# Performance work log

Measured on AMD Instinct MI355X. Metric: run time of the kernel, lower is better.

Reference implementation:

```python
import jax, jax.numpy as jnp
import numpy as np

B, S, E = 2, 4096, 2560
H, HKV, D = 8, 4, 256
WINDOW = 1024
SOFTCAP = 50.0
SCALING = 256.0 ** -0.5  # query_pre_attn_scalar = 256
EPS = 1e-6
MASK_VAL = -2.3819763e38


def rms_norm(x, w):
    # RMSNorm with add_unit_offset=True, computed in float32
    xf = x.astype(jnp.float32)
    out = xf * jax.lax.rsqrt(jnp.mean(xf * xf, axis=-1, keepdims=True) + EPS)
    return (out * (1.0 + w.astype(jnp.float32))).astype(x.dtype)


def apply_rotary_emb(x, cos, sin):
    # x: [B, S, h, D]; cos/sin: [S, D/2]; half-split rotation
    x1, x2 = jnp.split(x, 2, axis=-1)
    c = cos[None, :, None, :]
    s = sin[None, :, None, :]
    return jnp.concatenate([x1 * c - x2 * s, x2 * c + x1 * s], axis=-1)


def setup_inputs() -> dict:
    key = jax.random.key(0)
    ks = jax.random.split(key, 6)
    hidden_states = jax.random.normal(ks[0], (B, S, E), dtype=jnp.float32)
    # RoPE frequencies, theta=10000
    inv_freq = 1.0 / (10000.0 ** (np.arange(0, D, 2, dtype=np.float32) / D))
    t = np.arange(S, dtype=np.float32)
    freqs = np.outer(t, inv_freq)  # [S, D/2]
    freqs_cos = jnp.asarray(np.cos(freqs), dtype=jnp.float32)
    freqs_sin = jnp.asarray(np.sin(freqs), dtype=jnp.float32)
    kv_write_indices = jnp.arange(S, dtype=jnp.int32)
    k_cache = jnp.zeros((B, S, HKV, D), dtype=jnp.float32)
    v_cache = jnp.zeros((B, S, HKV, D), dtype=jnp.float32)
    # causal mask and causal+sliding-window mask (additive)
    i = np.arange(S)[:, None]
    j = np.arange(S)[None, :]
    causal = j <= i
    sliding = causal & ((i - j) < WINDOW)
    mask = jnp.asarray(np.where(causal, 0.0, MASK_VAL), dtype=jnp.float32)
    mask = jnp.broadcast_to(mask[None, None], (B, 1, S, S))
    local_mask = jnp.asarray(np.where(sliding, 0.0, MASK_VAL), dtype=jnp.float32)
    local_mask = jnp.broadcast_to(local_mask[None, None], (B, 1, S, S))
    w_qkv = jax.random.normal(ks[1], ((H + 2 * HKV) * D, E), dtype=jnp.float32) * (E ** -0.5)
    w_o = jax.random.normal(ks[2], (E, H * D), dtype=jnp.float32) * ((H * D) ** -0.5)
    q_norm_w = jnp.zeros((D,), dtype=jnp.float32)
    k_norm_w = jnp.zeros((D,), dtype=jnp.float32)
    return dict(hidden_states=hidden_states, freqs_cos=freqs_cos, freqs_sin=freqs_sin,
                kv_write_indices=kv_write_indices, k_cache=k_cache, v_cache=v_cache,
                mask=mask, local_mask=local_mask, w_qkv=w_qkv, w_o=w_o,
                q_norm_w=q_norm_w, k_norm_w=k_norm_w)


def reference(hidden_states, freqs_cos, freqs_sin, kv_write_indices, k_cache, v_cache,
              mask, local_mask, w_qkv, w_o, q_norm_w, k_norm_w):
    bsz, input_len, _ = hidden_states.shape
    qkv = jnp.einsum('bse,fe->bsf', hidden_states, w_qkv)
    xq, xk, xv = jnp.split(qkv, [H * D, H * D + HKV * D], axis=-1)
    xq = xq.reshape(bsz, input_len, H, D)
    xk = xk.reshape(bsz, input_len, HKV, D)
    xv = xv.reshape(bsz, input_len, HKV, D)
    # QK RMSNorm
    xq = rms_norm(xq, q_norm_w)
    xk = rms_norm(xk, k_norm_w)
    # RoPE
    xq = apply_rotary_emb(xq, freqs_cos, freqs_sin)
    xk = apply_rotary_emb(xk, freqs_cos, freqs_sin)
    # KV cache write
    k_cache = k_cache.at[:, kv_write_indices].set(xk)
    v_cache = v_cache.at[:, kv_write_indices].set(xv)
    kv_len = k_cache.shape[1]
    # GQA expand: [B, T, HKV, D] -> [B, T, H, D]
    nrep = H // HKV
    key = jnp.repeat(k_cache, nrep, axis=2)
    value = jnp.repeat(v_cache, nrep, axis=2)
    q = jnp.transpose(xq, (0, 2, 1, 3)) * SCALING   # [B, H, S, D]
    k = jnp.transpose(key, (0, 2, 1, 3))            # [B, H, T, D]
    v = jnp.transpose(value, (0, 2, 1, 3))
    scores = jnp.einsum('bhqd,bhkd->bhqk', q, k)
    # logit softcapping
    scores = jnp.tanh(scores / SOFTCAP) * SOFTCAP
    # attn_type == LOCAL_SLIDING -> use local (sliding-window) mask
    scores = scores + local_mask
    probs = jax.nn.softmax(scores.astype(jnp.float32), axis=-1).astype(q.dtype)
    out = jnp.einsum('bhqk,bhkd->bhqd', probs, v)
    out = jnp.transpose(out, (0, 2, 1, 3)).reshape(bsz, input_len, H * D)
    return jnp.einsum('bsf,ef->bse', out, w_o)
```

## Files before the change

kernel.cpp:

```cpp
#include <hip/hip_runtime.h>
#include <stdint.h>
#include <stddef.h>

#define B_    2
#define S_    4096
#define E_    2560
#define H_    8
#define HKV_  4
#define D_    256
#define F_    4096
#define HD_   2048
#define WIN_  1024

typedef __bf16 bf16;
typedef bf16  bf16x8 __attribute__((ext_vector_type(8)));
typedef bf16  bf16x4 __attribute__((ext_vector_type(4)));
typedef float f32x4  __attribute__((ext_vector_type(4)));
typedef uint32_t u32;

__device__ __forceinline__ void gl_lds16(const void* g, void* l) {
  __builtin_amdgcn_global_load_lds((const __attribute__((address_space(1))) void*)g,
                                   (__attribute__((address_space(3))) void*)l, 16, 0, 0);
}

__device__ __forceinline__ void bar_mf() {
  asm volatile("" ::: "memory");
  __builtin_amdgcn_s_barrier();
  asm volatile("" ::: "memory");
}

__device__ __forceinline__ u32 pkbf16(float a, float b) {
  union { bf16 h[2]; u32 u; } cv;
  cv.h[0] = (bf16)a; cv.h[1] = (bf16)b; return cv.u;
}

__global__ __launch_bounds__(256) void to_bf16_plain(const float* __restrict__ src,
                                                     bf16* __restrict__ dst, int n) {
  const int i = (blockIdx.x * 256 + threadIdx.x) * 8;
  if (i >= n) return;
  f32x4 a = *(const f32x4*)(src + i);
  f32x4 b = *(const f32x4*)(src + i + 4);
  bf16x8 o;
#pragma unroll
  for (int j = 0; j < 4; ++j) { o[j] = (bf16)a[j]; o[j + 4] = (bf16)b[j]; }
  *(bf16x8*)(dst + i) = o;
}

template <int EPI, int BN>
__global__ __launch_bounds__(512, 2) void gemm_8ph(
    const bf16* __restrict__ A, const bf16* __restrict__ Bw, int Kd, int NT,
    bf16* __restrict__ qo, bf16* __restrict__ ko, bf16* __restrict__ vto,
    float* __restrict__ C, int Nout, int row_base) {
  constexpr int NBH = BN / 128;
  constexpr int JT  = BN / 64;
  __shared__ bf16 Lds[2][2 + NBH][128 * 64];

  const int tid  = threadIdx.x;
  const int lane = tid & 63;
  const int wave = tid >> 6;
  const int wm   = wave >> 2;
  const int wn   = wave & 3;
  const int l16  = lane & 15;
  const int quad = lane >> 4;

  const int nwg  = gridDim.x * gridDim.y;
  const int obid = blockIdx.y * gridDim.x + blockIdx.x;
  const int bid  = (obid & 7) * (nwg >> 3) + (obid >> 3);
  const int mt   = bid / gridDim.x;
  const int ntl  = bid - mt * gridDim.x;
  const int row0 = mt * 256, col0 = ntl * BN;

  const bf16* Ah[2] = {A + (size_t)row0 * Kd, A + (size_t)(row0 + 128) * Kd};
  const bf16* Bh[2] = {Bw + (size_t)col0 * Kd,
                       Bw + (size_t)(col0 + (NBH == 2 ? 128 : 0)) * Kd};

  auto stage = [&](int dbf, int hf, const bf16* src, int k0) {
#pragma unroll
    for (int i = 0; i < 2; ++i) {
      const int g = tid + i * 512;
      const int r = g >> 3, c = g & 7;
      gl_lds16(src + (size_t)r * Kd + k0 + ((c ^ (r & 7)) << 3),
               &Lds[dbf][hf][0] + g * 8);
    }
  };
  auto rdA = [&](int dbf, int i, int ks) -> bf16x8 {
    const int r = i * 16 + l16;
    return *(const bf16x8*)&Lds[dbf][wm][r * 64 + (((ks * 4 + quad) ^ (r & 7)) << 3)];
  };
  auto rdB = [&](int dbf, int j, int ks) -> bf16x8 {
    const int colt = wn * (BN / 4) + j * 16 + l16;
    const int r = colt & 127;
    return *(const bf16x8*)&Lds[dbf][2 + (colt >> 7)][r * 64 + (((ks * 4 + quad) ^ (r & 7)) << 3)];
  };

  f32x4 acc[8][JT] = {};

  stage(0, 0, Ah[0], 0); stage(0, 1, Ah[1], 0);
#pragma unroll
  for (int h = 0; h < NBH; ++h) stage(0, 2 + h, Bh[h], 0);
  if (NT > 1) {
#pragma unroll
    for (int h = 0; h < NBH; ++h) stage(1, 2 + h, Bh[h], 64);
  }
  if constexpr (NBH == 2) asm volatile("s_waitcnt vmcnt(4)" ::: "memory");
  else                    asm volatile("s_waitcnt vmcnt(2)" ::: "memory");
  bar_mf();

  int db = 0;
  for (int t = 0; t < NT; ++t, db ^= 1) {
    const int k1 = (t + 1) * 64, k2 = (t + 2) * 64;
    const bool st1 = (t + 1 < NT), st2 = (t + 2 < NT);

    bf16x8 bfr[JT][2], a[4][2], a2[4][2];
#pragma unroll
    for (int j = 0; j < JT; ++j) { bfr[j][0] = rdB(db, j, 0); bfr[j][1] = rdB(db, j, 1); }
#pragma unroll
    for (int i = 0; i < 4; ++i) { a[i][0] = rdA(db, i, 0); a[i][1] = rdA(db, i, 1); }
    if (st1) stage(db ^ 1, 0, Ah[0], k1);
    bar_mf();
    __builtin_amdgcn_s_setprio(1);
#pragma unroll
    for (int i = 0; i < 2; ++i)
#pragma unroll
      for (int j = 0; j < JT; ++j) {
        acc[i][j] = __builtin_amdgcn_mfma_f32_16x16x32_bf16(a[i][0], bfr[j][0], acc[i][j], 0, 0, 0);
        acc[i][j] = __builtin_amdgcn_mfma_f32_16x16x32_bf16(a[i][1], bfr[j][1], acc[i][j], 0, 0, 0);
      }
    __builtin_amdgcn_s_setprio(0);
    bar_mf();

#pragma unroll
    for (int i = 0; i < 4; ++i) { a2[i][0] = rdA(db, i + 4, 0); a2[i][1] = rdA(db, i + 4, 1); }
    if (st1) stage(db ^ 1, 1, Ah[1], k1);
    bar_mf();
    __builtin_amdgcn_s_setprio(1);
#pragma unroll
    for (int i = 2; i < 4; ++i)
#pragma unroll
      for (int j = 0; j < JT; ++j) {
        acc[i][j] = __builtin_amdgcn_mfma_f32_16x16x32_bf16(a[i][0], bfr[j][0], acc[i][j], 0, 0, 0);
        acc[i][j] = __builtin_amdgcn_mfma_f32_16x16x32_bf16(a[i][1], bfr[j][1], acc[i][j], 0, 0, 0);
      }
    __builtin_amdgcn_s_setprio(0);
    bar_mf();

    if (st2) stage(db, 2, Bh[0], k2);
    bar_mf();
    __builtin_amdgcn_s_setprio(1);
#pragma unroll
    for (int i = 0; i < 2; ++i)
#pragma unroll
      for (int j = 0; j < JT; ++j) {
        acc[i + 4][j] = __builtin_amdgcn_mfma_f32_16x16x32_bf16(a2[i][0], bfr[j][0], acc[i + 4][j], 0, 0, 0);
        acc[i + 4][j] = __builtin_amdgcn_mfma_f32_16x16x32_bf16(a2[i][1], bfr[j][1], acc[i + 4][j], 0, 0, 0);
      }
    __builtin_amdgcn_s_setprio(0);
    bar_mf();

    if constexpr (NBH == 2) { if (st2) stage(db, 3, Bh[1], k2); }
    bar_mf();
    __builtin_amdgcn_s_setprio(1);
#pragma unroll
    for (int i = 2; i < 4; ++i)
#pragma unroll
      for (int j = 0; j < JT; ++j) {
        acc[i + 4][j] = __builtin_amdgcn_mfma_f32_16x16x32_bf16(a2[i][0], bfr[j][0], acc[i + 4][j], 0, 0, 0);
        acc[i + 4][j] = __builtin_amdgcn_mfma_f32_16x16x32_bf16(a2[i][1], bfr[j][1], acc[i + 4][j], 0, 0, 0);
      }
    __builtin_amdgcn_s_setprio(0);
    if (st2) {
      if constexpr (NBH == 2) asm volatile("s_waitcnt vmcnt(4)" ::: "memory");
      else                    asm volatile("s_waitcnt vmcnt(2)" ::: "memory");
    } else {
      asm volatile("s_waitcnt vmcnt(0)" ::: "memory");
    }
    bar_mf();
  }

#pragma unroll
  for (int i = 0; i < 8; ++i) {
    const int rbase = row_base + row0 + wm * 128 + i * 16 + quad * 4;
#pragma unroll
    for (int j = 0; j < JT; ++j) {
      const int c = col0 + wn * (BN / 4) + j * 16 + l16;
      if constexpr (EPI == 1) {
        int head = c >> 8;
        const int d = c & 255;
        if (head < 12) {
          bf16* base; int nh;
          if (head < 8) { base = qo; nh = H_; }
          else          { base = ko; nh = HKV_; head -= 8; }
#pragma unroll
          for (int rr = 0; rr < 4; ++rr) {
            const int row = rbase + rr;
            const int bb = row >> 12, s = row & 4095;
            base[(((size_t)(bb * nh + head) * S_) + s) * D_ + d] = (bf16)acc[i][j][rr];
          }
        } else {
          const int kh = head - 12;
          const int bb = rbase >> 12, s0 = rbase & 4095;
          bf16x4 pk;
#pragma unroll
          for (int rr = 0; rr < 4; ++rr) pk[rr] = (bf16)acc[i][j][rr];
          *(bf16x4*)(vto + (((size_t)(bb * HKV_ + kh) * D_ + d) * S_ + s0)) = pk;
        }
      } else {
#pragma unroll
        for (int rr = 0; rr < 4; ++rr)
          C[(size_t)(rbase + rr) * Nout + c] = acc[i][j][rr];
      }
    }
  }
}

__global__ __launch_bounds__(192) void normrope2(
    bf16* __restrict__ q, bf16* __restrict__ k,
    const float* __restrict__ fcos, const float* __restrict__ fsin,
    const int* __restrict__ widx,
    const float* __restrict__ qnw, const float* __restrict__ knw) {
  const int bx  = blockIdx.x;
  const int b   = bx >> 12;
  const int s   = bx & 4095;
  const int tid = threadIdx.x;
  const int hh  = tid >> 4;
  const int g   = tid & 15;
  const int d0  = g * 16;

  const bool isq = (hh < 8);
  bf16* rowp = isq ? (q + (((size_t)(b * H_ + hh) * S_ + s) * D_ + d0))
                   : (k + (((size_t)(b * HKV_ + (hh - 8)) * S_ + s) * D_ + d0));
  float x[16];
  {
    bf16x8 v0 = *(const bf16x8*)rowp;
    bf16x8 v1 = *(const bf16x8*)(rowp + 8);
#pragma unroll
    for (int i = 0; i < 8; ++i) { x[i] = (float)v0[i]; x[i + 8] = (float)v1[i]; }
  }

  float ssq = 0.f;
#pragma unroll
  for (int i = 0; i < 16; ++i) ssq += x[i] * x[i];
#pragma unroll
  for (int off = 1; off < 16; off <<= 1) ssq += __shfl_xor(ssq, off);
  const float sc = rsqrtf(ssq * (1.0f / 256.0f) + 1e-6f);
  const float* w = isq ? qnw : knw;
#pragma unroll
  for (int i = 0; i < 16; ++i) x[i] = x[i] * sc * (1.0f + w[d0 + i]);

  const int fbase = (g < 8) ? d0 : (d0 - 128);
  const float* cp = fcos + (size_t)s * 128 + fbase;
  const float* sp = fsin + (size_t)s * 128 + fbase;
#pragma unroll
  for (int i = 0; i < 16; ++i) {
    const float c = cp[i], sn = sp[i];
    const float other = __shfl_xor(x[i], 8);
    x[i] = (g < 8) ? (x[i] * c - other * sn)
                   : (x[i] * c + other * sn);
  }
  if (isq) {
#pragma unroll
    for (int i = 0; i < 16; ++i) x[i] *= 0.0625f;
  }

  bf16x8 o0, o1;
#pragma unroll
  for (int i = 0; i < 8; ++i) { o0[i] = (bf16)x[i]; o1[i] = (bf16)x[i + 8]; }

  bf16* dstp = isq ? rowp
                   : (k + (((size_t)(b * HKV_ + (hh - 8)) * S_ + widx[s]) * D_ + d0));
  *(bf16x8*)dstp = o0;
  *(bf16x8*)(dstp + 8) = o1;
}

__global__ __launch_bounds__(256) void attn_mfma(const bf16* __restrict__ Q,
                                                 const bf16* __restrict__ K,
                                                 const bf16* __restrict__ Vt,
                                                 bf16* __restrict__ out) {
  __shared__ bf16 Ks[2][32 * 256];
  __shared__ bf16 Vs[2][256 * 32];

  const int hw  = blockIdx.x;
  const int lid = (hw & 7) * 128 + (hw >> 3);
  const int bx  = lid & 63;
  const int bh  = lid >> 6;
  const int b   = bh >> 3, h = bh & 7, kh = h >> 1;

  const int lane = threadIdx.x & 63;
  const int wave = threadIdx.x >> 6;
  const int l16  = lane & 15;
  const int qd   = lane >> 4;
  const int swz  = l16 & 7;

  const int q0w = bx * 64 + wave * 16;
  const int iq  = q0w + l16;

  const bf16* Kb = K  + ((size_t)(b * HKV_ + kh) * S_) * D_;
  const bf16* Vb = Vt + ((size_t)(b * HKV_ + kh) * D_) * S_;

  bf16x8 qf[8];
  {
    const bf16* qp = Q + (((size_t)(b * H_ + h) * S_ + iq) * D_) + qd * 8;
#pragma unroll
    for (int kc = 0; kc < 8; ++kc) qf[kc] = *(const bf16x8*)(qp + kc * 32);
  }

  f32x4 Od[16] = {};
  float lsum = 0.f;

  int lo = bx * 64 - (WIN_ - 1); if (lo < 0) lo = 0;
  lo &= ~31;
  const int t1 = bx * 64 + 32;

  auto stage = [&](int buf, int kt) {
#pragma unroll
    for (int i = 0; i < 4; ++i) {
      const int r0  = wave * 8 + i * 2;
      const int row = r0 + (lane >> 5);
      const int c   = lane & 31;
      const int pk = (((row >> 2) & 3) << 3) + ((row >> 4) << 2) + (row & 3);
      gl_lds16(Kb + (size_t)(kt + pk) * D_ + ((c ^ (row & 7)) * 8),
               &Ks[buf][r0 * 256] + lane * 8);
    }
#pragma unroll
    for (int i = 0; i < 4; ++i) {
      const int d0 = (wave * 4 + i) * 16;
      const int d  = d0 + (lane >> 2);
      gl_lds16(Vb + (size_t)d * S_ + kt + (lane & 3) * 8,
               &Vs[buf][d0 * 32] + lane * 8);
    }
  };

  stage(0, lo);
  int buf = 0;

  const float c1 = 0.05770780163555853f;
  const float c2 = -144.26950408889634f;

  for (int kt = lo; kt <= t1; kt += 32) {
    const bool pre = (kt + 32 <= t1);
    if (pre) {
      stage(buf ^ 1, kt + 32);
      asm volatile("s_waitcnt vmcnt(8)" ::: "memory");
    } else {
      asm volatile("s_waitcnt vmcnt(0)" ::: "memory");
    }
    __builtin_amdgcn_s_barrier();
    asm volatile("" ::: "memory");

    const bool dead = (kt > q0w + 15) || (kt + 31 < q0w - (WIN_ - 1));
    if (!dead) {
      f32x4 sacc[2] = {};
#pragma unroll
      for (int kc = 0; kc < 8; ++kc) {
        const int ch = ((kc * 4 + qd) ^ swz) * 8;
        bf16x8 k0 = *(const bf16x8*)&Ks[buf][l16 * 256 + ch];
        bf16x8 k1 = *(const bf16x8*)&Ks[buf][(l16 + 16) * 256 + ch];
        sacc[0] = __builtin_amdgcn_mfma_f32_16x16x32_bf16(k0, qf[kc], sacc[0], 0, 0, 0);
        sacc[1] = __builtin_amdgcn_mfma_f32_16x16x32_bf16(k1, qf[kc], sacc[1], 0, 0, 0);
      }

      const bool interior = (kt + 31 <= q0w) && (kt >= q0w - 1008);
      const int  kb0 = kt + qd * 8;
      float p[8];
#pragma unroll
      for (int t = 0; t < 2; ++t)
#pragma unroll
        for (int r = 0; r < 4; ++r) {
          const float x = sacc[t][r];
          const float wv = __builtin_amdgcn_rcpf(exp2f(x * c1) + 1.0f);
          float pp = exp2f(c2 * wv);
          if (!interior) {
            const int key = kb0 + t * 4 + r;
            pp = (key <= iq && (iq - key) < WIN_) ? pp : 0.f;
          }
          p[t * 4 + r] = pp;
          lsum += pp;
        }

      union { u32 u[4]; bf16x8 v; } pf;
      pf.u[0] = pkbf16(p[0], p[1]);
      pf.u[1] = pkbf16(p[2], p[3]);
      pf.u[2] = pkbf16(p[4], p[5]);
      pf.u[3] = pkbf16(p[6], p[7]);

#pragma unroll
      for (int dt = 0; dt < 16; ++dt) {
        bf16x8 vf = *(const bf16x8*)&Vs[buf][(dt * 16 + l16) * 32 + qd * 8];
        Od[dt] = __builtin_amdgcn_mfma_f32_16x16x32_bf16(vf, pf.v, Od[dt], 0, 0, 0);
      }
    }

    asm volatile("" ::: "memory");
    __builtin_amdgcn_s_barrier();
    buf ^= 1;
  }

  float l = lsum + __shfl_xor(lsum, 16);
  l += __shfl_xor(l, 32);
  const float inv = 1.f / l;
  bf16* op = out + ((size_t)b * S_ + iq) * HD_ + h * D_ + qd * 4;
#pragma unroll
  for (int dt = 0; dt < 16; ++dt) {
    bf16x4 o4;
#pragma unroll
    for (int r = 0; r < 4; ++r) o4[r] = (bf16)(Od[dt][r] * inv);
    *(bf16x4*)(op + dt * 16) = o4;
  }
}

extern "C" void kernel_launch(void* const* d_in, const int* in_sizes, int n_in,
                              void* d_out, int out_size, void* d_ws, size_t ws_size,
                              hipStream_t stream) {
  const float* hidden = (const float*)d_in[0];
  const float* fcos   = (const float*)d_in[1];
  const float* fsin   = (const float*)d_in[2];
  const int*   widx   = (const int*)d_in[3];
  const float* wqkv   = (const float*)d_in[8];
  const float* wo     = (const float*)d_in[9];
  const float* qnw    = (const float*)d_in[10];
  const float* knw    = (const float*)d_in[11];
  float* out = (float*)d_out;

  char* ws = (char*)d_ws;
  const size_t MB = 1024 * 1024;
  const bool big = ws_size >= 126 * MB;

  bf16* wb_bf = (bf16*)(ws);
  bf16* hb_bf = (bf16*)(ws + 20 * MB);
  bf16* q_ws  = (bf16*)(ws + (big ? 60 : 32) * MB);
  bf16* k_ws  = (bf16*)(ws + (big ? 92 : 64) * MB);
  bf16* vt_ws = (bf16*)(ws + (big ? 108 : 80) * MB);
  bf16* att_o = (bf16*)(ws);
  bf16* wo_bf = (bf16*)(ws + 32 * MB);

  to_bf16_plain<<<(F_ * E_ / 8 + 255) / 256, 256, 0, stream>>>(wqkv, wb_bf, F_ * E_);

  const int nch   = big ? 1 : 4;
  const int chrow = (B_ * S_) / nch;
  for (int c = 0; c < nch; ++c) {
    const int row_base = c * chrow;
    to_bf16_plain<<<(chrow * E_ / 8 + 255) / 256, 256, 0, stream>>>(
        hidden + (size_t)row_base * E_, hb_bf, chrow * E_);
    if (big)
      gemm_8ph<1, 256><<<dim3(F_ / 256, chrow / 256), 512, 0, stream>>>(
          hb_bf, wb_bf, E_, E_ / 64, q_ws, k_ws, vt_ws, nullptr, 0, row_base);
    else
      gemm_8ph<1, 128><<<dim3(F_ / 128, chrow / 256), 512, 0, stream>>>(
          hb_bf, wb_bf, E_, E_ / 64, q_ws, k_ws, vt_ws, nullptr, 0, row_base);
  }

  normrope2<<<dim3(B_ * S_), 192, 0, stream>>>(q_ws, k_ws, fcos, fsin, widx, qnw, knw);
  attn_mfma<<<dim3(1024), 256, 0, stream>>>(q_ws, k_ws, vt_ws, att_o);
  to_bf16_plain<<<(E_ * HD_ / 8 + 255) / 256, 256, 0, stream>>>(wo, wo_bf, E_ * HD_);
  gemm_8ph<0, 128><<<dim3(E_ / 128, (B_ * S_) / 256), 512, 0, stream>>>(
      att_o, wo_bf, HD_, HD_ / 64, nullptr, nullptr, nullptr, out, E_, 0);
  (void)in_sizes; (void)n_in; (void)out_size;
}
```

Baseline: 809.9 us.

## Restructure GEMM K-loop to cut barriers and interleave LDS reads with MFMA

Reorganizes the inner K-loop of the bf16 MFMA GEMM so that A fragments are read in smaller pairs interleaved with compute. Both A-half stages for the next tile are issued up front, and both B-half stages for the tile after are issued together after a single barrier. This drops most of the per-iteration workgroup barriers to reduce sync stalls and improve overlap. The cost is a different ordering of LDS reads against asynchronous global-to-LDS writes. That ordering must stay hazard-free, because the B stage into buffer db now happens while A rows 6-7 are still being read from that same buffer.

```diff
diff --git a/kernel.cpp b/kernel.cpp
--- a/kernel.cpp
+++ b/kernel.cpp
@@ -111,63 +111,66 @@
     const int k1 = (t + 1) * 64, k2 = (t + 2) * 64;
     const bool st1 = (t + 1 < NT), st2 = (t + 2 < NT);
 
-    bf16x8 bfr[JT][2], a[4][2], a2[4][2];
+    bf16x8 bfr[JT][2], a01[2][2], a23[2][2], a45[2][2], a67[2][2];
 #pragma unroll
     for (int j = 0; j < JT; ++j) { bfr[j][0] = rdB(db, j, 0); bfr[j][1] = rdB(db, j, 1); }
 #pragma unroll
-    for (int i = 0; i < 4; ++i) { a[i][0] = rdA(db, i, 0); a[i][1] = rdA(db, i, 1); }
-    if (st1) stage(db ^ 1, 0, Ah[0], k1);
+    for (int i = 0; i < 2; ++i) { a01[i][0] = rdA(db, i, 0);     a01[i][1] = rdA(db, i, 1); }
+#pragma unroll
+    for (int i = 0; i < 2; ++i) { a23[i][0] = rdA(db, i + 2, 0); a23[i][1] = rdA(db, i + 2, 1); }
+    if (st1) { stage(db ^ 1, 0, Ah[0], k1); stage(db ^ 1, 1, Ah[1], k1); }
+
+    __builtin_amdgcn_s_setprio(1);
+#pragma unroll
+    for (int i = 0; i < 2; ++i)
+#pragma unroll
+      for (int j = 0; j < JT; ++j) {
+        acc[i][j] = __builtin_amdgcn_mfma_f32_16x16x32_bf16(a01[i][0], bfr[j][0], acc[i][j], 0, 0, 0);
+        acc[i][j] = __builtin_amdgcn_mfma_f32_16x16x32_bf16(a01[i][1], bfr[j][1], acc[i][j], 0, 0, 0);
+      }
+    __builtin_amdgcn_s_setprio(0);
+
+#pragma unroll
+    for (int i = 0; i < 2; ++i) { a45[i][0] = rdA(db, i + 4, 0); a45[i][1] = rdA(db, i + 4, 1); }
+
+    __builtin_amdgcn_s_setprio(1);
+#pragma unroll
+    for (int i = 0; i < 2; ++i)
+#pragma unroll
+      for (int j = 0; j < JT; ++j) {
+        acc[i + 2][j] = __builtin_amdgcn_mfma_f32_16x16x32_bf16(a23[i][0], bfr[j][0], acc[i + 2][j], 0, 0, 0);
+        acc[i + 2][j] = __builtin_amdgcn_mfma_f32_16x16x32_bf16(a23[i][1], bfr[j][1], acc[i + 2][j], 0, 0, 0);
+      }
+    __builtin_amdgcn_s_setprio(0);
+
     bar_mf();
+    if (st2) {
+      stage(db, 2, Bh[0], k2);
+      if constexpr (NBH == 2) stage(db, 3, Bh[1], k2);
+    }
+#pragma unroll
+    for (int i = 0; i < 2; ++i) { a67[i][0] = rdA(db, i + 6, 0); a67[i][1] = rdA(db, i + 6, 1); }
+
     __builtin_amdgcn_s_setprio(1);
 #pragma unroll
     for (int i = 0; i < 2; ++i)
 #pragma unroll
       for (int j = 0; j < JT; ++j) {
-        acc[i][j] = __builtin_amdgcn_mfma_f32_16x16x32_bf16(a[i][0], bfr[j][0], acc[i][j], 0, 0, 0);
-        acc[i][j] = __builtin_amdgcn_mfma_f32_16x16x32_bf16(a[i][1], bfr[j][1], acc[i][j], 0, 0, 0);
+        acc[i + 4][j] = __builtin_amdgcn_mfma_f32_16x16x32_bf16(a45[i][0], bfr[j][0], acc[i + 4][j], 0, 0, 0);
+        acc[i + 4][j] = __builtin_amdgcn_mfma_f32_16x16x32_bf16(a45[i][1], bfr[j][1], acc[i + 4][j], 0, 0, 0);
       }
     __builtin_amdgcn_s_setprio(0);
-    bar_mf();
-
-#pragma unroll
-    for (int i = 0; i < 4; ++i) { a2[i][0] = rdA(db, i + 4, 0); a2[i][1] = rdA(db, i + 4, 1); }
-    if (st1) stage(db ^ 1, 1, Ah[1], k1);
-    bar_mf();
+
     __builtin_amdgcn_s_setprio(1);
 #pragma unroll
-    for (int i = 2; i < 4; ++i)
+    for (int i = 0; i < 2; ++i)
 #pragma unroll
       for (int j = 0; j < JT; ++j) {
-        acc[i][j] = __builtin_amdgcn_mfma_f32_16x16x32_bf16(a[i][0], bfr[j][0], acc[i][j], 0, 0, 0);
-        acc[i][j] = __builtin_amdgcn_mfma_f32_16x16x32_bf16(a[i][1], bfr[j][1], acc[i][j], 0, 0, 0);
+        acc[i + 6][j] = __builtin_amdgcn_mfma_f32_16x16x32_bf16(a67[i][0], bfr[j][0], acc[i + 6][j], 0, 0, 0);
+        acc[i + 6][j] = __builtin_amdgcn_mfma_f32_16x16x32_bf16(a67[i][1], bfr[j][1], acc[i + 6][j], 0, 0, 0);
       }
     __builtin_amdgcn_s_setprio(0);
-    bar_mf();
-
-    if (st2) stage(db, 2, Bh[0], k2);
-    bar_mf();
-    __builtin_amdgcn_s_setprio(1);
-#pragma unroll
-    for (int i = 0; i < 2; ++i)
-#pragma unroll
-      for (int j = 0; j < JT; ++j) {
-        acc[i + 4][j] = __builtin_amdgcn_mfma_f32_16x16x32_bf16(a2[i][0], bfr[j][0], acc[i + 4][j], 0, 0, 0);
-        acc[i + 4][j] = __builtin_amdgcn_mfma_f32_16x16x32_bf16(a2[i][1], bfr[j][1], acc[i + 4][j], 0, 0, 0);
-      }
-    __builtin_amdgcn_s_setprio(0);
-    bar_mf();
-
-    if constexpr (NBH == 2) { if (st2) stage(db, 3, Bh[1], k2); }
-    bar_mf();
-    __builtin_amdgcn_s_setprio(1);
-#pragma unroll
-    for (int i = 2; i < 4; ++i)
-#pragma unroll
-      for (int j = 0; j < JT; ++j) {
-        acc[i + 4][j] = __builtin_amdgcn_mfma_f32_16x16x32_bf16(a2[i][0], bfr[j][0], acc[i + 4][j], 0, 0, 0);
-        acc[i + 4][j] = __builtin_amdgcn_mfma_f32_16x16x32_bf16(a2[i][1], bfr[j][1], acc[i + 4][j], 0, 0, 0);
-      }
-    __builtin_amdgcn_s_setprio(0);
+
     if (st2) {
       if constexpr (NBH == 2) asm volatile("s_waitcnt vmcnt(4)" ::: "memory");
       else                    asm volatile("s_waitcnt vmcnt(2)" ::: "memory");
```

After: 797.3 us. Within noise of the previous version (-1.6%).
